# Optimization experiments

Measured on AMD Instinct MI355X. Metric: run time of the kernel, lower is better.

Reference implementation:

```python
import jax, jax.numpy as jnp
import numpy as np

TEMP = 40.0
POOL = 7          # pooling_resolution
EPS = 1e-5


def setup_inputs() -> dict:
    key = jax.random.key(0)
    ks = jax.random.split(key, 16)
    B, C, H, W = 64, 512, 28, 28
    K = 7                      # kernel_size
    Cb = C // 4                # bottleneck channels
    P2 = POOL * POOL
    inp = {}
    inp["x"] = jax.random.normal(ks[0], (B, C, H, W), dtype=jnp.float32)
    # BatchNorm2d (eval mode: running stats + affine)
    inp["bn_gamma"] = 1.0 + 0.1 * jax.random.normal(ks[1], (C,), dtype=jnp.float32)
    inp["bn_beta"] = 0.1 * jax.random.normal(ks[2], (C,), dtype=jnp.float32)
    inp["bn_mean"] = 0.1 * jax.random.normal(ks[3], (C,), dtype=jnp.float32)
    inp["bn_var"] = jax.random.uniform(ks[4], (C,), minval=0.5, maxval=1.5, dtype=jnp.float32)
    # 1x1 conv weights (no bias)
    inp["Wq"] = jax.random.normal(ks[5], (C, C), dtype=jnp.float32) / np.sqrt(C)
    inp["Wk"] = jax.random.normal(ks[6], (C, C), dtype=jnp.float32) / np.sqrt(C)
    # kernel_layer: Linear(P^2 -> K^2, bias=False); torch weight shape (out,in)
    inp["Wkern"] = jax.random.normal(ks[7], (K * K, P2), dtype=jnp.float32) / np.sqrt(P2)
    # fusion_conv0: 1x1 conv C -> Cb, with bias
    inp["Wf0"] = jax.random.normal(ks[8], (Cb, C), dtype=jnp.float32) / np.sqrt(C)
    inp["bf0"] = 0.1 * jax.random.normal(ks[9], (Cb,), dtype=jnp.float32)
    # LayerNorm([Cb, K, K]) affine
    inp["ln_w"] = 1.0 + 0.1 * jax.random.normal(ks[10], (Cb, K, K), dtype=jnp.float32)
    inp["ln_b"] = 0.1 * jax.random.normal(ks[11], (Cb, K, K), dtype=jnp.float32)
    # fusion_conv1: 1x1 conv Cb -> C, with bias
    inp["Wf1"] = jax.random.normal(ks[12], (C, Cb), dtype=jnp.float32) / np.sqrt(Cb)
    inp["bf1"] = 0.1 * jax.random.normal(ks[13], (C,), dtype=jnp.float32)
    return inp


def reference(x, bn_gamma, bn_beta, bn_mean, bn_var, Wq, Wk, Wkern,
              Wf0, bf0, ln_w, ln_b, Wf1, bf1):
    B, C, H, W = x.shape
    K = int(round(Wkern.shape[0] ** 0.5))

    # AdaptiveAvgPool2d to (POOL, POOL); H, W divisible by POOL
    pooled = x.reshape(B, C, POOL, H // POOL, POOL, W // POOL).mean(axis=(3, 5))
    # BatchNorm2d (eval mode)
    pooled = (pooled - bn_mean[:, None, None]) * (
        bn_gamma[:, None, None] / jnp.sqrt(bn_var[:, None, None] + EPS)
    ) + bn_beta[:, None, None]

    pf = pooled.reshape(B, C, POOL * POOL)            # b c p
    Q = jnp.einsum('oc,bcp->bop', Wq, pf)             # b c p
    Kt = jnp.einsum('oc,bcp->bpo', Wk, pf)            # b p c
    attn = jax.nn.softmax(jnp.einsum('bcp,bpd->bcd', Q, Kt) / TEMP, axis=2)  # b c c

    kw = jnp.einsum('kp,bcp->bck', Wkern, pf)         # b c k^2
    kw = jnp.einsum('bcd,bdk->bck', attn, kw)         # b c k^2
    kw = kw.reshape(B, C, K, K)

    # fusion_conv0 (1x1) + LayerNorm([Cb,K,K]) + tanh + fusion_conv1 (1x1)
    kw = jnp.einsum('oc,bckl->bokl', Wf0, kw) + bf0[:, None, None]
    mu = kw.mean(axis=(1, 2, 3), keepdims=True)
    var = kw.var(axis=(1, 2, 3), keepdims=True)
    kw = (kw - mu) / jnp.sqrt(var + EPS) * ln_w + ln_b
    kw = jnp.tanh(kw)
    kw = jnp.einsum('oc,bckl->bokl', Wf1, kw) + bf1[:, None, None]  # b C K K

    # dynamic depthwise conv: one kernel per (b, c); groups = B*C
    weights = kw.reshape(B * C, 1, K, K)
    out = jax.lax.conv_general_dilated(
        x.reshape(1, B * C, H, W), weights,
        window_strides=(1, 1), padding=[(K // 2, K // 2)] * 2,
        feature_group_count=B * C,
        dimension_numbers=('NCHW', 'OIHW', 'NCHW'))
    return out.reshape(B, C, H, W)
```

## Files before the change

### kernel.cpp

```cpp
#include <hip/hip_runtime.h>
#include <math.h>

#define BB   64
#define CC   512
#define P2   49
#define CB   128
#define NB   3136
#define TEMPI (1.0f/40.0f)

typedef __attribute__((ext_vector_type(4))) short    bf16x4;
typedef __attribute__((ext_vector_type(4))) float    f32x4;
typedef unsigned short u16;

__device__ inline u16 f2bf(float f) {
    union { float f; unsigned u; } x{f};
    unsigned r = (x.u + 0x7FFFu + ((x.u >> 16) & 1u)) >> 16;
    return (u16)r;
}

__device__ inline f32x4 mfma16x16(bf16x4 a, bf16x4 b, f32x4 c) {
#if __has_builtin(__builtin_amdgcn_mfma_f32_16x16x16bf16_1k)
    return __builtin_amdgcn_mfma_f32_16x16x16bf16_1k(a, b, c, 0, 0, 0);
#elif __has_builtin(__builtin_amdgcn_mfma_f32_16x16x16_bf16)
    return __builtin_amdgcn_mfma_f32_16x16x16_bf16(a, b, c, 0, 0, 0);
#else
    f32x4 d;
    asm("v_mfma_f32_16x16x16_bf16 %0, %1, %2, %3"
        : "=v"(d) : "v"(a), "v"(b), "v"(c));
    return d;
#endif
}

__global__ __launch_bounds__(256) void pool_bn_k(
    const float* __restrict__ x, const float* __restrict__ g,
    const float* __restrict__ be, const float* __restrict__ mu,
    const float* __restrict__ var, float* __restrict__ pfT)
{
    int idx = blockIdx.x * 256 + threadIdx.x;
    int p  = idx % 49;
    int bc = idx / 49;
    int c  = bc & 511;
    int b  = bc >> 9;
    int py = p / 7, px = p % 7;
    const float* base = x + (size_t)bc * 784 + py * 4 * 28 + px * 4;
    float s = 0.f;
#pragma unroll
    for (int r = 0; r < 4; ++r) {
        float4 v = *(const float4*)(base + r * 28);
        s += v.x + v.y + v.z + v.w;
    }
    s *= (1.f / 16.f);
    float sc = g[c] * rsqrtf(var[c] + 1e-5f);
    pfT[(size_t)c * NB + b * 49 + p] = (s - mu[c]) * sc + be[c];
}

__global__ __launch_bounds__(256) void repack_pf_k(
    const float* __restrict__ pfT, u16* __restrict__ dst)
{
    int i = blockIdx.x * 256 + threadIdx.x;
    int l  = i & 63;
    int q  = (i >> 6) & 3;
    int ct = (i >> 8) & 31;
    int b  = i >> 13;
    int p  = q * 16 + (l & 15);
    int c0 = ct * 16 + ((l >> 4) << 2);
    ushort4 u;
    if (p < 49) {
        const float* s = pfT + (size_t)c0 * NB + b * 49 + p;
        u.x = f2bf(s[0]); u.y = f2bf(s[NB]);
        u.z = f2bf(s[2 * NB]); u.w = f2bf(s[3 * NB]);
    } else {
        u.x = u.y = u.z = u.w = 0;
    }
    ((ushort4*)dst)[i] = u;
}

__global__ __launch_bounds__(256) void repack_w_k(
    const float* __restrict__ W, u16* __restrict__ dst, int K)
{
    int i = blockIdx.x * 256 + threadIdx.x;
    int l  = i & 63;
    int KT = K >> 4;
    int ct = (i >> 6) % KT;
    int t  = (i >> 6) / KT;
    int o  = t * 16 + (l & 15);
    int c0 = ct * 16 + ((l >> 4) << 2);
    float4 v = *(const float4*)(W + (size_t)o * K + c0);
    ushort4 u;
    u.x = f2bf(v.x); u.y = f2bf(v.y); u.z = f2bf(v.z); u.w = f2bf(v.w);
    ((ushort4*)dst)[i] = u;
}

__global__ __launch_bounds__(256) void gemm_frag_k(
    const u16* __restrict__ pfF, const u16* __restrict__ WF,
    u16* __restrict__ dstF)
{
    int tid  = threadIdx.x;
    int lane = tid & 63;
    int w    = tid >> 6;
    int b    = blockIdx.y;
    int t    = blockIdx.x * 4 + w;

    const bf16x4* Ab = (const bf16x4*)pfF + (size_t)b * 8192 + lane;
    const bf16x4* Bw = (const bf16x4*)WF + (size_t)t * 2048 + lane;

    f32x4 acc[4];
#pragma unroll
    for (int q = 0; q < 4; ++q) acc[q] = (f32x4)0.f;

#pragma unroll
    for (int ct = 0; ct < 32; ++ct) {
        bf16x4 wv = Bw[ct * 64];
        bf16x4 a0 = Ab[(ct * 4 + 0) * 64];
        bf16x4 a1 = Ab[(ct * 4 + 1) * 64];
        bf16x4 a2 = Ab[(ct * 4 + 2) * 64];
        bf16x4 a3 = Ab[(ct * 4 + 3) * 64];
        acc[0] = mfma16x16(a0, wv, acc[0]);
        acc[1] = mfma16x16(a1, wv, acc[1]);
        acc[2] = mfma16x16(a2, wv, acc[2]);
        acc[3] = mfma16x16(a3, wv, acc[3]);
    }

#pragma unroll
    for (int q = 0; q < 4; ++q) {
        ushort4 u;
        u.x = f2bf(acc[q][0]); u.y = f2bf(acc[q][1]);
        u.z = f2bf(acc[q][2]); u.w = f2bf(acc[q][3]);
        ((ushort4*)dstF)[(((size_t)b * 32 + t) * 4 + q) * 64 + lane] = u;
    }
}

template <int KT>
__global__ __launch_bounds__(256) void fusion_frag_k(
    const u16* __restrict__ AF, const u16* __restrict__ WF,
    float* __restrict__ Cout, const float* __restrict__ bias)
{
    int tid  = threadIdx.x;
    int lane = tid & 63;
    int w    = tid >> 6;
    int b    = blockIdx.y;
    int t    = blockIdx.x * 4 + w;

    const bf16x4* Ab = (const bf16x4*)AF + (size_t)b * (KT * 256) + lane;
    const bf16x4* Bw = (const bf16x4*)WF + (size_t)t * (KT * 64) + lane;

    f32x4 acc[4];
#pragma unroll
    for (int q = 0; q < 4; ++q) acc[q] = (f32x4)0.f;

#pragma unroll
    for (int ct = 0; ct < KT; ++ct) {
        bf16x4 wv = Bw[ct * 64];
        bf16x4 a0 = Ab[(ct * 4 + 0) * 64];
        bf16x4 a1 = Ab[(ct * 4 + 1) * 64];
        bf16x4 a2 = Ab[(ct * 4 + 2) * 64];
        bf16x4 a3 = Ab[(ct * 4 + 3) * 64];
        acc[0] = mfma16x16(a0, wv, acc[0]);
        acc[1] = mfma16x16(a1, wv, acc[1]);
        acc[2] = mfma16x16(a2, wv, acc[2]);
        acc[3] = mfma16x16(a3, wv, acc[3]);
    }

    int c = t * 16 + (lane & 15);
    float bb = bias[c];
    float* op = Cout + (size_t)c * NB + b * 49;
    int g4 = (lane >> 4) << 2;
#pragma unroll
    for (int q = 0; q < 4; ++q) {
#pragma unroll
        for (int r = 0; r < 4; ++r) {
            int p = q * 16 + g4 + r;
            if (p < 49) op[p] = acc[q][r] + bb;
        }
    }
}

__global__ __launch_bounds__(256) void kwv_k(
    const float* __restrict__ pfT, const float* __restrict__ Wkern,
    u16* __restrict__ Vt)
{
    __shared__ float wk[2401];
    for (int l = threadIdx.x; l < 2401; l += 256) wk[l] = Wkern[l];
    __syncthreads();
    int idx = blockIdx.x * 256 + threadIdx.x;
    int k  = idx % 49;
    int cb = idx / 49;
    int base = (cb >> 6) * NB + (cb & 63) * 49;
    float s = 0.f;
#pragma unroll
    for (int p = 0; p < 49; ++p)
        s = fmaf(pfT[base + p], wk[k * 49 + p], s);
    Vt[base + k] = f2bf(s);
}

__global__ __launch_bounds__(256) void repack_v_k(
    const u16* __restrict__ src, u16* __restrict__ dst)
{
    int i = blockIdx.x * 256 + threadIdx.x;
    int l = i & 63;
    int pt = (i >> 6) & 3;
    int t = (i >> 8) & 31;
    int b = i >> 13;
    int p = pt * 16 + (l & 15);
    int d0 = t * 16 + ((l >> 4) << 2);
    ushort4 u;
    if (p < 49) {
        const u16* s = src + (size_t)d0 * NB + b * 49 + p;
        u.x = s[0]; u.y = s[NB]; u.z = s[2 * NB]; u.w = s[3 * NB];
    } else {
        u.x = u.y = u.z = u.w = 0;
    }
    ((ushort4*)dst)[i] = u;
}

__global__ __launch_bounds__(256) void attn_mfma_k(
    const u16* __restrict__ QF, const u16* __restrict__ KF,
    const u16* __restrict__ VF, u16* __restrict__ OtF)
{
    int tid  = threadIdx.x;
    int lane = tid & 63;
    int w    = tid >> 6;
    int b    = blockIdx.y;
    int ct   = blockIdx.x * 4 + w;

    const bf16x4* QFp = (const bf16x4*)QF + (size_t)b * 8192 + ct * 256 + lane;
    const bf16x4* KFp = (const bf16x4*)KF + (size_t)b * 8192 + lane;
    const bf16x4* VFp = (const bf16x4*)VF + (size_t)b * 8192 + lane;

    bf16x4 qf[4];
#pragma unroll
    for (int q = 0; q < 4; ++q) qf[q] = QFp[q * 64];

    f32x4 o[4];
#pragma unroll
    for (int pt = 0; pt < 4; ++pt) o[pt] = (f32x4)0.f;
    float lsum = 0.f;

    bf16x4 kf[4], vf[4], kn[4], vn[4];
#pragma unroll
    for (int q = 0; q < 4; ++q) { kf[q] = KFp[q * 64]; vf[q] = VFp[q * 64]; }

    for (int t = 0; t < 32; ++t) {
        if (t < 31) {
            const bf16x4* kp = KFp + (t + 1) * 256;
            const bf16x4* vp = VFp + (t + 1) * 256;
#pragma unroll
            for (int q = 0; q < 4; ++q) { kn[q] = kp[q * 64]; vn[q] = vp[q * 64]; }
        }
        f32x4 s = (f32x4)0.f;
#pragma unroll
        for (int q = 0; q < 4; ++q) s = mfma16x16(kf[q], qf[q], s);

        bf16x4 pa;
#pragma unroll
        for (int r = 0; r < 4; ++r) {
            float pe = __expf(s[r] * TEMPI);
            lsum += pe;
            pa[r] = (short)f2bf(pe);
        }
#pragma unroll
        for (int pt = 0; pt < 4; ++pt) o[pt] = mfma16x16(pa, vf[pt], o[pt]);

#pragma unroll
        for (int q = 0; q < 4; ++q) { kf[q] = kn[q]; vf[q] = vn[q]; }
    }

    lsum += __shfl_xor(lsum, 16);
    lsum += __shfl_xor(lsum, 32);
    float linv = 1.f / lsum;

    int g4 = (lane >> 4) << 2;
    float rl0 = __shfl(linv, g4 + 0);
    float rl1 = __shfl(linv, g4 + 1);
    float rl2 = __shfl(linv, g4 + 2);
    float rl3 = __shfl(linv, g4 + 3);

#pragma unroll
    for (int pt = 0; pt < 4; ++pt) {
        ushort4 u;
        u.x = f2bf(o[pt][0] * rl0);
        u.y = f2bf(o[pt][1] * rl1);
        u.z = f2bf(o[pt][2] * rl2);
        u.w = f2bf(o[pt][3] * rl3);
        ((ushort4*)OtF)[(((size_t)b * 32 + ct) * 4 + pt) * 64 + lane] = u;
    }
}

__global__ __launch_bounds__(256) void ln_tanh_k(
    const float* __restrict__ F0, const float* __restrict__ lnw,
    const float* __restrict__ lnb, u16* __restrict__ GF)
{
    int b = blockIdx.x, tid = threadIdx.x;
    float s = 0.f, sq = 0.f;
    for (int e = tid; e < CB * 49; e += 256) {
        int o = e / 49, k = e - o * 49;
        float v = F0[o * NB + b * 49 + k];
        s += v; sq += v * v;
    }
#pragma unroll
    for (int off = 32; off > 0; off >>= 1) {
        s  += __shfl_xor(s, off);
        sq += __shfl_xor(sq, off);
    }
    __shared__ float rs[4], rq[4];
    __shared__ float smu, srstd;
    int wv = tid >> 6;
    if ((tid & 63) == 0) { rs[wv] = s; rq[wv] = sq; }
    __syncthreads();
    if (tid == 0) {
        float S = rs[0] + rs[1] + rs[2] + rs[3];
        float Q = rq[0] + rq[1] + rq[2] + rq[3];
        float mu = S / 6272.f;
        float v  = Q / 6272.f - mu * mu;
        smu = mu; srstd = rsqrtf(v + 1e-5f);
    }
    __syncthreads();
    float mu = smu, rstd = srstd;
    for (int e = tid; e < CB * 49; e += 256) {
        int o = e / 49, k = e - o * 49;
        float g = tanhf((F0[o * NB + b * 49 + k] - mu) * rstd * lnw[e] + lnb[e]);
        int ct = o >> 4, rr = o & 15;
        int l  = ((rr >> 2) << 4) | (k & 15);
        int q  = k >> 4;
        GF[((((size_t)b * 8 + ct) * 4 + q) * 64 + l) * 4 + (rr & 3)] = f2bf(g);
    }
    for (int e = tid; e < CB * 15; e += 256) {
        int o = e / 15, k = 49 + (e % 15);
        int ct = o >> 4, rr = o & 15;
        int l  = ((rr >> 2) << 4) | (k & 15);
        GF[((((size_t)b * 8 + ct) * 4 + 3) * 64 + l) * 4 + (rr & 3)] = 0;
    }
}

#define PLS 1256
__global__ __launch_bounds__(256) void dwconv_k(
    const float* __restrict__ x, const float* __restrict__ KernT,
    float* __restrict__ out)
{
    __shared__ float xs[4 * PLS];
    int tid  = threadIdx.x;
    int lane = tid & 63;
    int wid  = tid >> 6;
    int P    = blockIdx.x * 4 + wid;
    int b = P >> 9, c = P & 511;
    float* pl = &xs[wid * PLS];

    float4* plf = (float4*)pl;
#pragma unroll
    for (int r = 0; r < 5; ++r) {
        int l = lane + 64 * r;
        if (l < PLS / 4) plf[l] = float4{0.f, 0.f, 0.f, 0.f};
    }

    float wvl = 0.f;
    if (lane < 49) wvl = KernT[(size_t)c * NB + b * 49 + lane];
    int wvi = __float_as_int(wvl);
    float w[49];
#pragma unroll
    for (int i = 0; i < 49; ++i)
        w[i] = __int_as_float(__builtin_amdgcn_readlane(wvi, i));

    const float* src = x + (size_t)P * 784;
#pragma unroll
    for (int r = 0; r < 4; ++r) {
        int q = lane + 64 * r;
        if (q < 196) {
            int y = q / 7, xq = 4 * (q % 7);
            int R = y + 3;
            *(float4*)&pl[R * 36 + (((R >> 2) & 7) << 2) + xq + 4] =
                *(const float4*)(src + y * 28 + xq);
        }
    }

    if (lane >= 49) return;
    int ty = lane / 7, gx = lane - ty * 7;
    int y0 = 4 * ty, x0 = 4 * gx;
    float acc[4][4] = {};

#pragma unroll
    for (int yy = 0; yy < 10; ++yy) {
        int R = y0 + yy;
        const float* rp = &xs[wid * PLS + R * 36 + (((R >> 2) & 7) << 2) + x0];
        float4 fa = *(const float4*)(rp);
        float4 fb = *(const float4*)(rp + 4);
        float4 fc = *(const float4*)(rp + 8);
        float f[12] = {fa.x, fa.y, fa.z, fa.w, fb.x, fb.y, fb.z, fb.w,
                       fc.x, fc.y, fc.z, fc.w};
#pragma unroll
        for (int j = 0; j < 4; ++j) {
            int dy = yy - j;
            if (dy < 0 || dy > 6) continue;
#pragma unroll
            for (int dx = 0; dx < 7; ++dx) {
                float wv = w[dy * 7 + dx];
                acc[j][0] = fmaf(wv, f[dx + 1], acc[j][0]);
                acc[j][1] = fmaf(wv, f[dx + 2], acc[j][1]);
                acc[j][2] = fmaf(wv, f[dx + 3], acc[j][2]);
                acc[j][3] = fmaf(wv, f[dx + 4], acc[j][3]);
            }
        }
    }

    float* op = out + (size_t)P * 784;
#pragma unroll
    for (int j = 0; j < 4; ++j) {
        float4 o4 = {acc[j][0], acc[j][1], acc[j][2], acc[j][3]};
        *(float4*)(op + (y0 + j) * 28 + x0) = o4;
    }
}

extern "C" void kernel_launch(void* const* d_in, const int* in_sizes, int n_in,
                              void* d_out, int out_size, void* d_ws, size_t ws_size,
                              hipStream_t stream)
{
    const float* x     = (const float*)d_in[0];
    const float* bng   = (const float*)d_in[1];
    const float* bnb   = (const float*)d_in[2];
    const float* bnm   = (const float*)d_in[3];
    const float* bnv   = (const float*)d_in[4];
    const float* Wq    = (const float*)d_in[5];
    const float* Wk    = (const float*)d_in[6];
    const float* Wkern = (const float*)d_in[7];
    const float* Wf0   = (const float*)d_in[8];
    const float* bf0   = (const float*)d_in[9];
    const float* lnw   = (const float*)d_in[10];
    const float* lnb   = (const float*)d_in[11];
    const float* Wf1   = (const float*)d_in[12];
    const float* bf1   = (const float*)d_in[13];
    float* out = (float*)d_out;
    float* ws  = (float*)d_ws;

    float* pfT  = ws;
    u16*   pfF  = (u16*)(ws + 1605632);
    u16*   WqF  = (u16*)(ws + 2654208);
    u16*   WkF  = (u16*)(ws + 2785280);
    u16*   Wf0F = (u16*)(ws + 2916352);
    u16*   Wf1F = (u16*)(ws + 2949120);
    u16*   Vt   = (u16*)(ws + 2981888);
    u16*   QF   = (u16*)(ws + 3784704);
    u16*   KF   = (u16*)(ws + 4833280);
    u16*   VF   = (u16*)(ws + 5881856);
    u16*   OtF  = (u16*)ws;
    float* F0    = ws + 1605632;
    u16*   GF    = (u16*)(ws + 2007040);
    float* KernT = ws + 3784704;

    pool_bn_k<<<6272, 256, 0, stream>>>(x, bng, bnb, bnm, bnv, pfT);
    repack_pf_k<<<2048, 256, 0, stream>>>(pfT, pfF);
    repack_w_k<<<256, 256, 0, stream>>>(Wq, WqF, 512);
    repack_w_k<<<256, 256, 0, stream>>>(Wk, WkF, 512);
    repack_w_k<<<64, 256, 0, stream>>>(Wf0, Wf0F, 512);
    repack_w_k<<<64, 256, 0, stream>>>(Wf1, Wf1F, 128);
    kwv_k<<<6272, 256, 0, stream>>>(pfT, Wkern, Vt);
    gemm_frag_k<<<dim3(8, 64), 256, 0, stream>>>(pfF, WqF, QF);
    gemm_frag_k<<<dim3(8, 64), 256, 0, stream>>>(pfF, WkF, KF);
    repack_v_k<<<2048, 256, 0, stream>>>(Vt, VF);
    attn_mfma_k<<<dim3(8, 64), 256, 0, stream>>>(QF, KF, VF, OtF);
    fusion_frag_k<32><<<dim3(2, 64), 256, 0, stream>>>(OtF, Wf0F, F0, bf0);
    ln_tanh_k<<<64, 256, 0, stream>>>(F0, lnw, lnb, GF);
    fusion_frag_k<8><<<dim3(8, 64), 256, 0, stream>>>(GF, Wf1F, KernT, bf1);
    dwconv_k<<<8192, 256, 0, stream>>>(x, KernT, out);
}
```

Baseline: 196.2 us.

## Fuse pooling, repacks, kernel-weight GEMM and LayerNorm into fewer kernels

Cuts the launch sequence from about fifteen kernels to seven. Pool+BN, the pf repack and the Wkern projection are merged into one kernel that computes the Wkern step on MFMA from LDS. The four weight repacks become one launch, the Q and K GEMMs share a grid, and fusion_conv0 is fused with LayerNorm+tanh using LDS. The aim is to remove launch overhead and intermediate global round-trips, at the cost of lower parallelism in prep_k (256 blocks) and f0ln_k (64 blocks), plus extra bf16 rounding of the Wkern inputs.

```diff
diff --git a/kernel.cpp b/kernel.cpp
--- a/kernel.cpp
+++ b/kernel.cpp
@@ -31,70 +31,118 @@
 #endif
 }
 
-__global__ __launch_bounds__(256) void pool_bn_k(
-    const float* __restrict__ x, const float* __restrict__ g,
-    const float* __restrict__ be, const float* __restrict__ mu,
-    const float* __restrict__ var, float* __restrict__ pfT)
-{
-    int idx = blockIdx.x * 256 + threadIdx.x;
-    int p  = idx % 49;
-    int bc = idx / 49;
-    int c  = bc & 511;
-    int b  = bc >> 9;
-    int py = p / 7, px = p % 7;
-    const float* base = x + (size_t)bc * 784 + py * 4 * 28 + px * 4;
-    float s = 0.f;
-#pragma unroll
-    for (int r = 0; r < 4; ++r) {
-        float4 v = *(const float4*)(base + r * 28);
-        s += v.x + v.y + v.z + v.w;
-    }
-    s *= (1.f / 16.f);
-    float sc = g[c] * rsqrtf(var[c] + 1e-5f);
-    pfT[(size_t)c * NB + b * 49 + p] = (s - mu[c]) * sc + be[c];
-}
-
-__global__ __launch_bounds__(256) void repack_pf_k(
-    const float* __restrict__ pfT, u16* __restrict__ dst)
-{
-    int i = blockIdx.x * 256 + threadIdx.x;
-    int l  = i & 63;
-    int q  = (i >> 6) & 3;
-    int ct = (i >> 8) & 31;
-    int b  = i >> 13;
-    int p  = q * 16 + (l & 15);
-    int c0 = ct * 16 + ((l >> 4) << 2);
-    ushort4 u;
-    if (p < 49) {
-        const float* s = pfT + (size_t)c0 * NB + b * 49 + p;
-        u.x = f2bf(s[0]); u.y = f2bf(s[NB]);
-        u.z = f2bf(s[2 * NB]); u.w = f2bf(s[3 * NB]);
-    } else {
-        u.x = u.y = u.z = u.w = 0;
-    }
-    ((ushort4*)dst)[i] = u;
-}
-
-__global__ __launch_bounds__(256) void repack_w_k(
-    const float* __restrict__ W, u16* __restrict__ dst, int K)
-{
-    int i = blockIdx.x * 256 + threadIdx.x;
-    int l  = i & 63;
+__global__ __launch_bounds__(256) void repack_all_k(
+    const float* __restrict__ Wq, const float* __restrict__ Wk,
+    const float* __restrict__ Wf0, const float* __restrict__ Wf1,
+    const float* __restrict__ Wkern,
+    u16* __restrict__ WqF, u16* __restrict__ WkF,
+    u16* __restrict__ Wf0F, u16* __restrict__ Wf1F,
+    u16* __restrict__ WkernF)
+{
+    int u = blockIdx.x * 256 + threadIdx.x;
+    if (u >= 163840) {
+        int uu = u - 163840;
+        int l = uu & 63, rest = uu >> 6;
+        int ct = rest & 3, t = rest >> 2;
+        int o  = t * 16 + (l & 15);
+        int c0 = ct * 16 + ((l >> 4) << 2);
+        ushort4 v;
+        v.x = (o < 49 && c0 + 0 < 49) ? f2bf(Wkern[o * 49 + c0 + 0]) : 0;
+        v.y = (o < 49 && c0 + 1 < 49) ? f2bf(Wkern[o * 49 + c0 + 1]) : 0;
+        v.z = (o < 49 && c0 + 2 < 49) ? f2bf(Wkern[o * 49 + c0 + 2]) : 0;
+        v.w = (o < 49 && c0 + 3 < 49) ? f2bf(Wkern[o * 49 + c0 + 3]) : 0;
+        ((ushort4*)WkernF)[uu] = v;
+        return;
+    }
+    const float* W; u16* dst; int K, uu;
+    if (u < 65536)       { W = Wq;  dst = WqF;  K = 512; uu = u; }
+    else if (u < 131072) { W = Wk;  dst = WkF;  K = 512; uu = u - 65536; }
+    else if (u < 147456) { W = Wf0; dst = Wf0F; K = 512; uu = u - 131072; }
+    else                 { W = Wf1; dst = Wf1F; K = 128; uu = u - 147456; }
+    int l = uu & 63, rest = uu >> 6;
     int KT = K >> 4;
-    int ct = (i >> 6) % KT;
-    int t  = (i >> 6) / KT;
+    int ct = rest % KT, t = rest / KT;
     int o  = t * 16 + (l & 15);
     int c0 = ct * 16 + ((l >> 4) << 2);
     float4 v = *(const float4*)(W + (size_t)o * K + c0);
-    ushort4 u;
-    u.x = f2bf(v.x); u.y = f2bf(v.y); u.z = f2bf(v.z); u.w = f2bf(v.w);
-    ((ushort4*)dst)[i] = u;
-}
-
-__global__ __launch_bounds__(256) void gemm_frag_k(
-    const u16* __restrict__ pfF, const u16* __restrict__ WF,
-    u16* __restrict__ dstF)
-{
+    ushort4 w;
+    w.x = f2bf(v.x); w.y = f2bf(v.y); w.z = f2bf(v.z); w.w = f2bf(v.w);
+    ((ushort4*)dst)[uu] = w;
+}
+
+__global__ __launch_bounds__(256) void prep_k(
+    const float* __restrict__ x, const float* __restrict__ g,
+    const float* __restrict__ be, const float* __restrict__ mu,
+    const float* __restrict__ var, const u16* __restrict__ WkernF,
+    u16* __restrict__ pfF, u16* __restrict__ VF)
+{
+    __shared__ float pf[128][50];
+    int tid = threadIdx.x;
+    int bg  = blockIdx.x;
+    int b = bg >> 2, grp = bg & 3;
+    int cbase = grp * 128;
+
+    for (int i = tid; i < 128 * 49; i += 256) {
+        int cl = i / 49, p = i - cl * 49;
+        int c = cbase + cl;
+        const float* basep = x + ((size_t)(b * 512 + c)) * 784
+                             + (p / 7) * 4 * 28 + (p % 7) * 4;
+        float s = 0.f;
+#pragma unroll
+        for (int r = 0; r < 4; ++r) {
+            float4 v = *(const float4*)(basep + r * 28);
+            s += v.x + v.y + v.z + v.w;
+        }
+        s *= (1.f / 16.f);
+        float sc = g[c] * rsqrtf(var[c] + 1e-5f);
+        pf[cl][p] = (s - mu[c]) * sc + be[c];
+    }
+    __syncthreads();
+
+    for (int u = tid; u < 2048; u += 256) {
+        int l = u & 63, q = (u >> 6) & 3, ctl = u >> 8;
+        int p   = q * 16 + (l & 15);
+        int c0l = ctl * 16 + ((l >> 4) << 2);
+        ushort4 o;
+        if (p < 49) {
+            o.x = f2bf(pf[c0l + 0][p]); o.y = f2bf(pf[c0l + 1][p]);
+            o.z = f2bf(pf[c0l + 2][p]); o.w = f2bf(pf[c0l + 3][p]);
+        } else { o.x = o.y = o.z = o.w = 0; }
+        ((ushort4*)pfF)[((size_t)(b * 32 + grp * 8 + ctl) * 4 + q) * 64 + l] = o;
+    }
+
+    int lane = tid & 63, w = tid >> 6;
+    const bf16x4* WkF4 = (const bf16x4*)WkernF;
+#pragma unroll
+    for (int i = 0; i < 8; ++i) {
+        int dt  = w * 8 + i;
+        int ct2 = dt >> 2, tk = dt & 3;
+        int cc  = ct2 * 16 + (lane & 15);
+        f32x4 acc = (f32x4)0.f;
+#pragma unroll
+        for (int ptp = 0; ptp < 4; ++ptp) {
+            bf16x4 af;
+#pragma unroll
+            for (int j = 0; j < 4; ++j) {
+                int p = ptp * 16 + ((lane >> 4) << 2) + j;
+                af[j] = (short)((p < 49) ? f2bf(pf[cc][p]) : 0);
+            }
+            bf16x4 bw = WkF4[(tk * 4 + ptp) * 64 + lane];
+            acc = mfma16x16(af, bw, acc);
+        }
+        ushort4 o;
+        o.x = f2bf(acc[0]); o.y = f2bf(acc[1]);
+        o.z = f2bf(acc[2]); o.w = f2bf(acc[3]);
+        ((ushort4*)VF)[((size_t)(b * 32 + grp * 8 + ct2) * 4 + tk) * 64 + lane] = o;
+    }
+}
+
+__global__ __launch_bounds__(256) void gemm_qk_k(
+    const u16* __restrict__ pfF, const u16* __restrict__ WqF,
+    const u16* __restrict__ WkF, u16* __restrict__ QF, u16* __restrict__ KF)
+{
+    const u16* WF   = blockIdx.z ? WkF : WqF;
+    u16*       dstF = blockIdx.z ? KF : QF;
     int tid  = threadIdx.x;
     int lane = tid & 63;
     int w    = tid >> 6;
@@ -130,6 +178,161 @@
     }
 }
 
+__global__ __launch_bounds__(256) void attn_mfma_k(
+    const u16* __restrict__ QF, const u16* __restrict__ KF,
+    const u16* __restrict__ VF, u16* __restrict__ OtF)
+{
+    int tid  = threadIdx.x;
+    int lane = tid & 63;
+    int w    = tid >> 6;
+    int b    = blockIdx.y;
+    int ct   = blockIdx.x * 4 + w;
+
+    const bf16x4* QFp = (const bf16x4*)QF + (size_t)b * 8192 + ct * 256 + lane;
+    const bf16x4* KFp = (const bf16x4*)KF + (size_t)b * 8192 + lane;
+    const bf16x4* VFp = (const bf16x4*)VF + (size_t)b * 8192 + lane;
+
+    bf16x4 qf[4];
+#pragma unroll
+    for (int q = 0; q < 4; ++q) qf[q] = QFp[q * 64];
+
+    f32x4 o[4];
+#pragma unroll
+    for (int pt = 0; pt < 4; ++pt) o[pt] = (f32x4)0.f;
+    float lsum = 0.f;
+
+    bf16x4 kf[4], vf[4], kn[4], vn[4];
+#pragma unroll
+    for (int q = 0; q < 4; ++q) { kf[q] = KFp[q * 64]; vf[q] = VFp[q * 64]; }
+
+    for (int t = 0; t < 32; ++t) {
+        if (t < 31) {
+            const bf16x4* kp = KFp + (t + 1) * 256;
+            const bf16x4* vp = VFp + (t + 1) * 256;
+#pragma unroll
+            for (int q = 0; q < 4; ++q) { kn[q] = kp[q * 64]; vn[q] = vp[q * 64]; }
+        }
+        f32x4 s = (f32x4)0.f;
+#pragma unroll
+        for (int q = 0; q < 4; ++q) s = mfma16x16(kf[q], qf[q], s);
+
+        bf16x4 pa;
+#pragma unroll
+        for (int r = 0; r < 4; ++r) {
+            float pe = __expf(s[r] * TEMPI);
+            lsum += pe;
+            pa[r] = (short)f2bf(pe);
+        }
+#pragma unroll
+        for (int pt = 0; pt < 4; ++pt) o[pt] = mfma16x16(pa, vf[pt], o[pt]);
+
+#pragma unroll
+        for (int q = 0; q < 4; ++q) { kf[q] = kn[q]; vf[q] = vn[q]; }
+    }
+
+    lsum += __shfl_xor(lsum, 16);
+    lsum += __shfl_xor(lsum, 32);
+    float linv = 1.f / lsum;
+
+    int g4 = (lane >> 4) << 2;
+    float rl0 = __shfl(linv, g4 + 0);
+    float rl1 = __shfl(linv, g4 + 1);
+    float rl2 = __shfl(linv, g4 + 2);
+    float rl3 = __shfl(linv, g4 + 3);
+
+#pragma unroll
+    for (int pt = 0; pt < 4; ++pt) {
+        ushort4 u;
+        u.x = f2bf(o[pt][0] * rl0);
+        u.y = f2bf(o[pt][1] * rl1);
+        u.z = f2bf(o[pt][2] * rl2);
+        u.w = f2bf(o[pt][3] * rl3);
+        ((ushort4*)OtF)[(((size_t)b * 32 + ct) * 4 + pt) * 64 + lane] = u;
+    }
+}
+
+__global__ __launch_bounds__(512) void f0ln_k(
+    const u16* __restrict__ OtF, const u16* __restrict__ Wf0F,
+    const float* __restrict__ bf0, const float* __restrict__ lnw,
+    const float* __restrict__ lnb, u16* __restrict__ GF)
+{
+    __shared__ float F0[128][50];
+    __shared__ float rs[8], rq[8];
+    __shared__ float smu, srstd;
+    int tid  = threadIdx.x;
+    int lane = tid & 63, w = tid >> 6;
+    int b = blockIdx.x;
+
+    const bf16x4* Ab = (const bf16x4*)OtF + (size_t)b * 8192 + lane;
+    const bf16x4* Bw = (const bf16x4*)Wf0F + (size_t)w * 2048 + lane;
+
+    f32x4 acc[4];
+#pragma unroll
+    for (int q = 0; q < 4; ++q) acc[q] = (f32x4)0.f;
+#pragma unroll
+    for (int ct = 0; ct < 32; ++ct) {
+        bf16x4 wv = Bw[ct * 64];
+        bf16x4 a0 = Ab[(ct * 4 + 0) * 64];
+        bf16x4 a1 = Ab[(ct * 4 + 1) * 64];
+        bf16x4 a2 = Ab[(ct * 4 + 2) * 64];
+        bf16x4 a3 = Ab[(ct * 4 + 3) * 64];
+        acc[0] = mfma16x16(a0, wv, acc[0]);
+        acc[1] = mfma16x16(a1, wv, acc[1]);
+        acc[2] = mfma16x16(a2, wv, acc[2]);
+        acc[3] = mfma16x16(a3, wv, acc[3]);
+    }
+
+    int c = w * 16 + (lane & 15);
+    float bb = bf0[c];
+    int g4 = (lane >> 4) << 2;
+#pragma unroll
+    for (int q = 0; q < 4; ++q)
+#pragma unroll
+        for (int r = 0; r < 4; ++r) {
+            int p = q * 16 + g4 + r;
+            if (p < 49) F0[c][p] = acc[q][r] + bb;
+        }
+    __syncthreads();
+
+    float s = 0.f, sq = 0.f;
+    for (int e = tid; e < CB * 49; e += 512) {
+        int o = e / 49, k = e - o * 49;
+        float v = F0[o][k];
+        s += v; sq += v * v;
+    }
+#pragma unroll
+    for (int off = 32; off > 0; off >>= 1) {
+        s  += __shfl_xor(s, off);
+        sq += __shfl_xor(sq, off);
+    }
+    if ((tid & 63) == 0) { rs[w] = s; rq[w] = sq; }
+    __syncthreads();
+    if (tid == 0) {
+        float S = 0.f, Q = 0.f;
+#pragma unroll
+        for (int i = 0; i < 8; ++i) { S += rs[i]; Q += rq[i]; }
+        float mu = S / 6272.f;
+        float v  = Q / 6272.f - mu * mu;
+        smu = mu; srstd = rsqrtf(v + 1e-5f);
+    }
+    __syncthreads();
+    float mu = smu, rstd = srstd;
+
+    for (int u = tid; u < 2048; u += 512) {
+        int l = u & 63, q = (u >> 6) & 3, ct = u >> 8;
+        int c0 = ct * 16 + ((l >> 4) << 2);
+        int k  = q * 16 + (l & 15);
+        ushort4 o;
+        if (k < 49) {
+            o.x = f2bf(tanhf((F0[c0+0][k] - mu) * rstd * lnw[(c0+0)*49+k] + lnb[(c0+0)*49+k]));
+            o.y = f2bf(tanhf((F0[c0+1][k] - mu) * rstd * lnw[(c0+1)*49+k] + lnb[(c0+1)*49+k]));
+            o.z = f2bf(tanhf((F0[c0+2][k] - mu) * rstd * lnw[(c0+2)*49+k] + lnb[(c0+2)*49+k]));
+            o.w = f2bf(tanhf((F0[c0+3][k] - mu) * rstd * lnw[(c0+3)*49+k] + lnb[(c0+3)*49+k]));
+        } else { o.x = o.y = o.z = o.w = 0; }
+        ((ushort4*)GF)[(((size_t)b * 8 + ct) * 4 + q) * 64 + l] = o;
+    }
+}
+
 template <int KT>
 __global__ __launch_bounds__(256) void fusion_frag_k(
     const u16* __restrict__ AF, const u16* __restrict__ WF,
@@ -175,163 +378,6 @@
     }
 }
 
-__global__ __launch_bounds__(256) void kwv_k(
-    const float* __restrict__ pfT, const float* __restrict__ Wkern,
-    u16* __restrict__ Vt)
-{
-    __shared__ float wk[2401];
-    for (int l = threadIdx.x; l < 2401; l += 256) wk[l] = Wkern[l];
-    __syncthreads();
-    int idx = blockIdx.x * 256 + threadIdx.x;
-    int k  = idx % 49;
-    int cb = idx / 49;
-    int base = (cb >> 6) * NB + (cb & 63) * 49;
-    float s = 0.f;
-#pragma unroll
-    for (int p = 0; p < 49; ++p)
-        s = fmaf(pfT[base + p], wk[k * 49 + p], s);
-    Vt[base + k] = f2bf(s);
-}
-
-__global__ __launch_bounds__(256) void repack_v_k(
-    const u16* __restrict__ src, u16* __restrict__ dst)
-{
-    int i = blockIdx.x * 256 + threadIdx.x;
-    int l = i & 63;
-    int pt = (i >> 6) & 3;
-    int t = (i >> 8) & 31;
-    int b = i >> 13;
-    int p = pt * 16 + (l & 15);
-    int d0 = t * 16 + ((l >> 4) << 2);
-    ushort4 u;
-    if (p < 49) {
-        const u16* s = src + (size_t)d0 * NB + b * 49 + p;
-        u.x = s[0]; u.y = s[NB]; u.z = s[2 * NB]; u.w = s[3 * NB];
-    } else {
-        u.x = u.y = u.z = u.w = 0;
-    }
-    ((ushort4*)dst)[i] = u;
-}
-
-__global__ __launch_bounds__(256) void attn_mfma_k(
-    const u16* __restrict__ QF, const u16* __restrict__ KF,
-    const u16* __restrict__ VF, u16* __restrict__ OtF)
-{
-    int tid  = threadIdx.x;
-    int lane = tid & 63;
-    int w    = tid >> 6;
-    int b    = blockIdx.y;
-    int ct   = blockIdx.x * 4 + w;
-
-    const bf16x4* QFp = (const bf16x4*)QF + (size_t)b * 8192 + ct * 256 + lane;
-    const bf16x4* KFp = (const bf16x4*)KF + (size_t)b * 8192 + lane;
-    const bf16x4* VFp = (const bf16x4*)VF + (size_t)b * 8192 + lane;
-
-    bf16x4 qf[4];
-#pragma unroll
-    for (int q = 0; q < 4; ++q) qf[q] = QFp[q * 64];
-
-    f32x4 o[4];
-#pragma unroll
-    for (int pt = 0; pt < 4; ++pt) o[pt] = (f32x4)0.f;
-    float lsum = 0.f;
-
-    bf16x4 kf[4], vf[4], kn[4], vn[4];
-#pragma unroll
-    for (int q = 0; q < 4; ++q) { kf[q] = KFp[q * 64]; vf[q] = VFp[q * 64]; }
-
-    for (int t = 0; t < 32; ++t) {
-        if (t < 31) {
-            const bf16x4* kp = KFp + (t + 1) * 256;
-            const bf16x4* vp = VFp + (t + 1) * 256;
-#pragma unroll
-            for (int q = 0; q < 4; ++q) { kn[q] = kp[q * 64]; vn[q] = vp[q * 64]; }
-        }
-        f32x4 s = (f32x4)0.f;
-#pragma unroll
-        for (int q = 0; q < 4; ++q) s = mfma16x16(kf[q], qf[q], s);
-
-        bf16x4 pa;
-#pragma unroll
-        for (int r = 0; r < 4; ++r) {
-            float pe = __expf(s[r] * TEMPI);
-            lsum += pe;
-            pa[r] = (short)f2bf(pe);
-        }
-#pragma unroll
-        for (int pt = 0; pt < 4; ++pt) o[pt] = mfma16x16(pa, vf[pt], o[pt]);
-
-#pragma unroll
-        for (int q = 0; q < 4; ++q) { kf[q] = kn[q]; vf[q] = vn[q]; }
-    }
-
-    lsum += __shfl_xor(lsum, 16);
-    lsum += __shfl_xor(lsum, 32);
-    float linv = 1.f / lsum;
-
-    int g4 = (lane >> 4) << 2;
-    float rl0 = __shfl(linv, g4 + 0);
-    float rl1 = __shfl(linv, g4 + 1);
-    float rl2 = __shfl(linv, g4 + 2);
-    float rl3 = __shfl(linv, g4 + 3);
-
-#pragma unroll
-    for (int pt = 0; pt < 4; ++pt) {
-        ushort4 u;
-        u.x = f2bf(o[pt][0] * rl0);
-        u.y = f2bf(o[pt][1] * rl1);
-        u.z = f2bf(o[pt][2] * rl2);
-        u.w = f2bf(o[pt][3] * rl3);
-        ((ushort4*)OtF)[(((size_t)b * 32 + ct) * 4 + pt) * 64 + lane] = u;
-    }
-}
-
-__global__ __launch_bounds__(256) void ln_tanh_k(
-    const float* __restrict__ F0, const float* __restrict__ lnw,
-    const float* __restrict__ lnb, u16* __restrict__ GF)
-{
-    int b = blockIdx.x, tid = threadIdx.x;
-    float s = 0.f, sq = 0.f;
-    for (int e = tid; e < CB * 49; e += 256) {
-        int o = e / 49, k = e - o * 49;
-        float v = F0[o * NB + b * 49 + k];
-        s += v; sq += v * v;
-    }
-#pragma unroll
-    for (int off = 32; off > 0; off >>= 1) {
-        s  += __shfl_xor(s, off);
-        sq += __shfl_xor(sq, off);
-    }
-    __shared__ float rs[4], rq[4];
-    __shared__ float smu, srstd;
-    int wv = tid >> 6;
-    if ((tid & 63) == 0) { rs[wv] = s; rq[wv] = sq; }
-    __syncthreads();
-    if (tid == 0) {
-        float S = rs[0] + rs[1] + rs[2] + rs[3];
-        float Q = rq[0] + rq[1] + rq[2] + rq[3];
-        float mu = S / 6272.f;
-        float v  = Q / 6272.f - mu * mu;
-        smu = mu; srstd = rsqrtf(v + 1e-5f);
-    }
-    __syncthreads();
-    float mu = smu, rstd = srstd;
-    for (int e = tid; e < CB * 49; e += 256) {
-        int o = e / 49, k = e - o * 49;
-        float g = tanhf((F0[o * NB + b * 49 + k] - mu) * rstd * lnw[e] + lnb[e]);
-        int ct = o >> 4, rr = o & 15;
-        int l  = ((rr >> 2) << 4) | (k & 15);
-        int q  = k >> 4;
-        GF[((((size_t)b * 8 + ct) * 4 + q) * 64 + l) * 4 + (rr & 3)] = f2bf(g);
-    }
-    for (int e = tid; e < CB * 15; e += 256) {
-        int o = e / 15, k = 49 + (e % 15);
-        int ct = o >> 4, rr = o & 15;
-        int l  = ((rr >> 2) << 4) | (k & 15);
-        GF[((((size_t)b * 8 + ct) * 4 + 3) * 64 + l) * 4 + (rr & 3)] = 0;
-    }
-}
-
 #define PLS 1256
 __global__ __launch_bounds__(256) void dwconv_k(
     const float* __restrict__ x, const float* __restrict__ KernT,
@@ -380,7 +426,7 @@
 #pragma unroll
     for (int yy = 0; yy < 10; ++yy) {
         int R = y0 + yy;
-        const float* rp = &xs[wid * PLS + R * 36 + (((R >> 2) & 7) << 2) + x0];
+        const float* rp = &pl[R * 36 + (((R >> 2) & 7) << 2) + x0];
         float4 fa = *(const float4*)(rp);
         float4 fb = *(const float4*)(rp + 4);
         float4 fc = *(const float4*)(rp + 8);
@@ -430,34 +476,25 @@
     float* out = (float*)d_out;
     float* ws  = (float*)d_ws;
 
-    float* pfT  = ws;
-    u16*   pfF  = (u16*)(ws + 1605632);
-    u16*   WqF  = (u16*)(ws + 2654208);
-    u16*   WkF  = (u16*)(ws + 2785280);
-    u16*   Wf0F = (u16*)(ws + 2916352);
-    u16*   Wf1F = (u16*)(ws + 2949120);
-    u16*   Vt   = (u16*)(ws + 2981888);
-    u16*   QF   = (u16*)(ws + 3784704);
-    u16*   KF   = (u16*)(ws + 4833280);
-    u16*   VF   = (u16*)(ws + 5881856);
-    u16*   OtF  = (u16*)ws;
-    float* F0    = ws + 1605632;
-    u16*   GF    = (u16*)(ws + 2007040);
-    float* KernT = ws + 3784704;
-
-    pool_bn_k<<<6272, 256, 0, stream>>>(x, bng, bnb, bnm, bnv, pfT);
-    repack_pf_k<<<2048, 256, 0, stream>>>(pfT, pfF);
-    repack_w_k<<<256, 256, 0, stream>>>(Wq, WqF, 512);
-    repack_w_k<<<256, 256, 0, stream>>>(Wk, WkF, 512);
-    repack_w_k<<<64, 256, 0, stream>>>(Wf0, Wf0F, 512);
-    repack_w_k<<<64, 256, 0, stream>>>(Wf1, Wf1F, 128);
-    kwv_k<<<6272, 256, 0, stream>>>(pfT, Wkern, Vt);
-    gemm_frag_k<<<dim3(8, 64), 256, 0, stream>>>(pfF, WqF, QF);
-    gemm_frag_k<<<dim3(8, 64), 256, 0, stream>>>(pfF, WkF, KF);
-    repack_v_k<<<2048, 256, 0, stream>>>(Vt, VF);
+    u16* pfF    = (u16*)(ws + 0);
+    u16* VF     = (u16*)(ws + 1048576);
+    u16* WqF    = (u16*)(ws + 2097152);
+    u16* WkF    = (u16*)(ws + 2228224);
+    u16* Wf0F   = (u16*)(ws + 2359296);
+    u16* Wf1F   = (u16*)(ws + 2392064);
+    u16* WkernF = (u16*)(ws + 2424832);
+    u16* QF     = (u16*)(ws + 2426880);
+    u16* KF     = (u16*)(ws + 3475456);
+    u16* OtF    = (u16*)(ws + 4524032);
+    u16* GF     = (u16*)(ws + 5572608);
+    float* KernT = ws + 2426880;
+
+    repack_all_k<<<644, 256, 0, stream>>>(Wq, Wk, Wf0, Wf1, Wkern,
+                                          WqF, WkF, Wf0F, Wf1F, WkernF);
+    prep_k<<<256, 256, 0, stream>>>(x, bng, bnb, bnm, bnv, WkernF, pfF, VF);
+    gemm_qk_k<<<dim3(8, 64, 2), 256, 0, stream>>>(pfF, WqF, WkF, QF, KF);
     attn_mfma_k<<<dim3(8, 64), 256, 0, stream>>>(QF, KF, VF, OtF);
-    fusion_frag_k<32><<<dim3(2, 64), 256, 0, stream>>>(OtF, Wf0F, F0, bf0);
-    ln_tanh_k<<<64, 256, 0, stream>>>(F0, lnw, lnb, GF);
+    f0ln_k<<<64, 512, 0, stream>>>(OtF, Wf0F, bf0, lnw, lnb, GF);
     fusion_frag_k<8><<<dim3(8, 64), 256, 0, stream>>>(GF, Wf1F, KernT, bf1);
     dwconv_k<<<8192, 256, 0, stream>>>(x, KernT, out);
 }
```

New measurement: 159.0 us (median of 2 runs). -18.9%, faster.
